# Optimization experiments

Hardware: AMD Instinct MI355X
Metric: run time of the kernel (lower is better)

## Reference

```python
import jax, jax.numpy as jnp
import numpy as np

N_BUILDINGS = 4096
NUM_CLUSTERS = 128
EMBED_DIM = 128
TEMPORAL_DIM = 24


def setup_inputs() -> dict:
    key = jax.random.key(0)
    ks = jax.random.split(key, 12)
    E, N, C, T = EMBED_DIM, N_BUILDINGS, NUM_CLUSTERS, TEMPORAL_DIM

    def lin(k, fi, fo):
        k1, k2 = jax.random.split(k)
        w = jax.random.normal(k1, (fo, fi), jnp.float32) / np.sqrt(fi).astype(np.float32)
        b = jax.random.normal(k2, (fo,), jnp.float32) * 0.01
        return w, b

    fp_w1, fp_b1 = lin(ks[0], 2 * E + 2, 128)
    fp_w2, fp_b2 = lin(ks[1], 128, 64)
    fp_w3, fp_b3 = lin(ks[2], 64, 1)
    en_w1, en_b1 = lin(ks[3], 1, 16)
    en_w2, en_b2 = lin(ks[4], 16, 1)
    ps_w1, ps_b1 = lin(ks[5], E, 32)
    ps_w2, ps_b2 = lin(ks[6], 32, 1)

    embeddings = jax.random.normal(ks[7], (1, N, E), jnp.float32)
    generation = jax.random.uniform(ks[8], (1, N, T), jnp.float32) * 50.0
    consumption = jax.random.uniform(ks[9], (1, N, T), jnp.float32) * 50.0
    positions = jax.random.uniform(ks[10], (1, N, 2), jnp.float32) * 1000.0
    cluster_assignments = (jnp.arange(N) % C)[None, :].astype(jnp.int32)

    return dict(embeddings=embeddings, generation=generation, consumption=consumption,
                positions=positions,
                fp_w1=fp_w1, fp_b1=fp_b1, fp_w2=fp_w2, fp_b2=fp_b2, fp_w3=fp_w3, fp_b3=fp_b3,
                en_w1=en_w1, en_b1=en_b1, en_w2=en_w2, en_b2=en_b2,
                ps_w1=ps_w1, ps_b1=ps_b1, ps_w2=ps_w2, ps_b2=ps_b2,
                cluster_assignments=cluster_assignments, num_clusters=C, current_hour=12)


def _greedy_cluster(net0, prio, effm, pf):
    """Greedy allocation within one cluster. net0,prio: [K]; effm,pf: [K,K].
    Surplus rows and deficit cols are both visited in descending priority order;
    non-surplus rows have avail=0 and non-deficit cols have needed<=0, matching the
    original code's subset selection + break/continue semantics."""
    K = net0.shape[0]
    order = jnp.argsort(-prio)
    inv = jnp.argsort(order)
    net_o = net0[order]
    eff_o = effm[order][:, order]
    pf_o = pf[order][:, order]

    def outer(dnet, i):
        avail0 = jnp.maximum(net_o[i], 0.0)  # surplus net is never mutated

        def inner(carry, j):
            avail, dn = carry
            needed = -dn[j]
            active = (avail > 0.0) & (needed > 0.0)
            f = jnp.where(active, jnp.minimum(jnp.minimum(avail, needed), pf_o[i, j]), 0.0)
            dn = dn.at[j].add(f * eff_o[i, j])  # deficit receives delivered flow
            return (avail - f, dn), (f, active)

        (_, dnet), (frow, arow) = jax.lax.scan(inner, (avail0, dnet), jnp.arange(K))
        return dnet, (frow, arow)

    dnet, (flows_o, act_o) = jax.lax.scan(outer, net_o, jnp.arange(K))
    return flows_o[inv][:, inv], act_o[inv][:, inv], dnet[inv]


def _forward(embeddings, generation, consumption, positions,
             fp_w1, fp_b1, fp_w2, fp_b2, fp_w3, fp_b3,
             en_w1, en_b1, en_w2, en_b2,
             ps_w1, ps_b1, ps_w2, ps_b2,
             cluster_assignments, num_clusters, current_hour):
    B, N, E = embeddings.shape
    C = num_clusters
    K = N // C
    net = generation[0, :, current_hour] - consumption[0, :, current_hour]  # [N]

    g = jnp.argsort(cluster_assignments[0]).reshape(C, K)  # [C,K] building ids per cluster
    emb_c = embeddings[0][g]   # [C,K,E]
    pos_c = positions[0][g]    # [C,K,2]
    net_c = net[g]             # [C,K]

    # priority scorer (eval mode)
    h = jax.nn.relu(emb_c @ ps_w1.T + ps_b1)
    prio_c = jax.nn.sigmoid(h @ ps_w2.T + ps_b2)[..., 0]  # [C,K]

    # pairwise distances within cluster
    dist = jnp.linalg.norm(pos_c[:, :, None, :] - pos_c[:, None, :, :], axis=-1)  # [C,K,K]

    # efficiency net: eff = 0.85 + 0.13*sigmoid(MLP(dist/1000))
    eh = jax.nn.relu((dist / 1000.0)[..., None] * en_w1[:, 0] + en_b1)  # [C,K,K,16]
    eff = 0.85 + 0.13 * jax.nn.sigmoid(eh @ en_w2.T + en_b2)[..., 0]    # [C,K,K]

    # flow predictor on concat([emb_i, emb_j, dist, hour/24]); split W1 to avoid
    # materializing the [C,K,K,2E+2] feature tensor. Dropout is eval-mode identity.
    W1a, W1b = fp_w1[:, :E], fp_w1[:, E:2 * E]
    w1d, w1h = fp_w1[:, 2 * E], fp_w1[:, 2 * E + 1]
    hi = emb_c @ W1a.T  # [C,K,128]
    hj = emb_c @ W1b.T  # [C,K,128]
    hour_f = current_hour / 24.0
    h1 = jax.nn.relu(hi[:, :, None, :] + hj[:, None, :, :] + dist[..., None] * w1d + hour_f * w1h + fp_b1)
    h2 = jax.nn.relu(h1 @ fp_w2.T + fp_b2)
    pflow = jax.nn.softplus(h2 @ fp_w3.T + fp_b3)[..., 0]  # [C,K,K]

    flows_c, act_c, dnet_c = jax.vmap(_greedy_cluster)(net_c, prio_c, eff, pflow)

    sharing = jnp.zeros((N, N), embeddings.dtype).at[g[:, :, None], g[:, None, :]].set(flows_c)
    effmat = jnp.ones((N, N), embeddings.dtype).at[g[:, :, None], g[:, None, :]].set(
        jnp.where(act_c, eff, 1.0))
    net_after = jnp.zeros((N,), embeddings.dtype).at[g].set(dnet_c)

    sharing = sharing[None]
    effmat = effmat[None]
    total_shared = sharing.sum()
    energy_sent = sharing.sum(axis=2)
    energy_received = (sharing * effmat).sum(axis=1)
    return sharing, effmat, total_shared, energy_sent, energy_received, net_after[None]


def reference(embeddings, generation, consumption, positions,
              fp_w1, fp_b1, fp_w2, fp_b2, fp_w3, fp_b3,
              en_w1, en_b1, en_w2, en_b2,
              ps_w1, ps_b1, ps_w2, ps_b2,
              cluster_assignments, num_clusters, current_hour):
    return _forward(embeddings, generation, consumption, positions,
                    fp_w1, fp_b1, fp_w2, fp_b2, fp_w3, fp_b3,
                    en_w1, en_b1, en_w2, en_b2,
                    ps_w1, ps_b1, ps_w2, ps_b2,
                    cluster_assignments, num_clusters, current_hour)
```

## Files before the change

### kernel.cpp

```cpp
#include <hip/hip_runtime.h>
#include <math.h>

#define NB 4096
#define NC 128
#define NK 32
#define NE 128

typedef __bf16 bf16x8 __attribute__((ext_vector_type(8)));
typedef float floatx4 __attribute__((ext_vector_type(4)));

__device__ __forceinline__ float sigmoidf_(float x){
  if (x >= 0.f){ float z = expf(-x); return 1.f/(1.f+z); }
  float z = expf(x); return z/(1.f+z);
}
__device__ __forceinline__ float softplusf_(float x){
  return fmaxf(x, 0.f) + log1pf(expf(-fabsf(x)));
}
__device__ __forceinline__ unsigned int pack_bf16(float a, float b){
  unsigned short ua = __builtin_bit_cast(unsigned short, (__bf16)a);
  unsigned short ub = __builtin_bit_cast(unsigned short, (__bf16)b);
  return (unsigned int)ua | ((unsigned int)ub << 16);
}

__global__ void k_prep_group(const float* __restrict__ fp_w1, const float* __restrict__ ps_w1,
                             const float* __restrict__ fp_b1, const float* __restrict__ fp_w2,
                             const int* __restrict__ assign, const int* __restrict__ hourp,
                             float* __restrict__ w1at, float* __restrict__ w1bt,
                             float* __restrict__ ps_w1t, int* __restrict__ g,
                             int* __restrict__ row_of, float* __restrict__ w1d_c,
                             float* __restrict__ bzc, uint4* __restrict__ w2f,
                             float* __restrict__ total){
  int bid = blockIdx.x;
  int t = threadIdx.x;
  if (bid < 80){
    int idx = bid*256 + t;
    if (idx < 128*128){
      int o = idx >> 7, e = idx & 127;
      w1at[e*128 + o] = fp_w1[o*258 + e];
      w1bt[e*128 + o] = fp_w1[o*258 + 128 + e];
    } else {
      int i2 = idx - 128*128;
      if (i2 < 128*32){
        int e = i2 >> 5, q = i2 & 31;
        ps_w1t[e*32 + q] = ps_w1[q*128 + e];
      }
    }
  } else if (bid < 96){
    __shared__ int hist[NC];
    __shared__ int loc[256];
    int start = (bid - 80)*256;
    for (int c = t; c < NC; c += 256) hist[c] = 0;
    __syncthreads();
    for (int j = t; j < start; j += 256) atomicAdd(&hist[assign[j]], 1);
    int i = start + t;
    int c = assign[i];
    loc[t] = c;
    __syncthreads();
    int r = hist[c];
    for (int j = 0; j < 256; ++j) r += (j < t && loc[j] == c) ? 1 : 0;
    if (r >= NK) r = NK - 1;
    g[c*NK + r] = i;
    row_of[i] = c*NK + r;
  } else if (bid == 96){
    if (t < 128){
      float hour_f = (float)hourp[0] / 24.0f;
      w1d_c[t] = fp_w1[t*258 + 256];
      bzc[t]   = fmaf(hour_f, fp_w1[t*258 + 257], fp_b1[t]);
    }
    if (t == 128) total[0] = 0.f;
  } else {
    for (int ff = t; ff < 1024; ff += 256){
      int lane = ff & 63, fi = ff >> 6;
      int nt = fi >> 2, ks = fi & 3;
      int o = nt*16 + (lane & 15);
      int kb = ks*32 + (lane >> 4)*8;
      const float* src = fp_w2 + o*128 + kb;
      uint4 u;
      u.x = pack_bf16(src[0], src[1]);
      u.y = pack_bf16(src[2], src[3]);
      u.z = pack_bf16(src[4], src[5]);
      u.w = pack_bf16(src[6], src[7]);
      w2f[ff] = u;
    }
  }
}

__global__ void k_prio(const float* __restrict__ emb, const float* __restrict__ gen,
                       const float* __restrict__ cons, const float* __restrict__ pos,
                       const float* __restrict__ ps_w1t, const float* __restrict__ ps_b1,
                       const float* __restrict__ ps_w2, const float* __restrict__ ps_b2,
                       const int* __restrict__ row_of, const int* __restrict__ hourp,
                       float* __restrict__ net_c, float* __restrict__ prio_c,
                       float* __restrict__ pos_c){
  __shared__ float es[8*128];
  __shared__ float ws[128*32];
  int t = threadIdx.x;
  int i0 = blockIdx.x*8;
  for (int idx = t; idx < 8*128; idx += 256) es[idx] = emb[i0*128 + idx];
  for (int idx = t; idx < 128*32; idx += 256) ws[idx] = ps_w1t[idx];
  __syncthreads();
  int bl = t >> 5, q = t & 31;
  int i = i0 + bl;
  float acc = ps_b1[q];
  const float* er = &es[bl*128];
  for (int e = 0; e < 128; ++e) acc = fmaf(er[e], ws[e*32 + q], acc);
  float v = fmaxf(acc, 0.f) * ps_w2[q];
  for (int m = 16; m >= 1; m >>= 1) v += __shfl_xor(v, m, 32);
  if (q == 0){
    int ck = row_of[i];
    prio_c[ck] = sigmoidf_(v + ps_b2[0]);
    int h = hourp[0];
    net_c[ck] = gen[i*24 + h] - cons[i*24 + h];
    pos_c[2*ck]   = pos[2*i];
    pos_c[2*ck+1] = pos[2*i+1];
  }
}

__global__ void k_hij(const float* __restrict__ emb, const float* __restrict__ w1at,
                      const float* __restrict__ w1bt, const int* __restrict__ row_of,
                      float* __restrict__ hi_c, float* __restrict__ hj_c){
  __shared__ float es[16*132];
  int t = threadIdx.x;
  int i0 = blockIdx.x*16;
  for (int idx = t; idx < 16*128; idx += 256){
    int b = idx >> 7, e = idx & 127;
    es[b*132 + e] = emb[(i0 + b)*128 + e];
  }
  __syncthreads();
  int o = t & 127, half = t >> 7;
  float ai[8], aj[8];
#pragma unroll
  for (int r = 0; r < 8; ++r){ ai[r] = 0.f; aj[r] = 0.f; }
  for (int e = 0; e < 128; e += 4){
    float wa0 = w1at[(e+0)*128 + o], wa1 = w1at[(e+1)*128 + o];
    float wa2 = w1at[(e+2)*128 + o], wa3 = w1at[(e+3)*128 + o];
    float wb0 = w1bt[(e+0)*128 + o], wb1 = w1bt[(e+1)*128 + o];
    float wb2 = w1bt[(e+2)*128 + o], wb3 = w1bt[(e+3)*128 + o];
#pragma unroll
    for (int r = 0; r < 8; ++r){
      float4 ev = *(const float4*)&es[(half*8 + r)*132 + e];
      ai[r] = fmaf(ev.x, wa0, fmaf(ev.y, wa1, fmaf(ev.z, wa2, fmaf(ev.w, wa3, ai[r]))));
      aj[r] = fmaf(ev.x, wb0, fmaf(ev.y, wb1, fmaf(ev.z, wb2, fmaf(ev.w, wb3, aj[r]))));
    }
  }
#pragma unroll
  for (int r = 0; r < 8; ++r){
    int b = i0 + half*8 + r;
    int ck = row_of[b];
    hi_c[ck*128 + o] = ai[r];
    hj_c[ck*128 + o] = aj[r];
  }
}

__global__ __launch_bounds__(256) void k_pflow(
    const float* __restrict__ hi_c, const float* __restrict__ hj_c,
    const float* __restrict__ pos_c, const float* __restrict__ w1d_c,
    const float* __restrict__ bzc, const uint4* __restrict__ w2f,
    const float* __restrict__ fp_b2, const float* __restrict__ fp_w3,
    const float* __restrict__ fp_b3, float* __restrict__ pflow){
  int t = threadIdx.x;
  int lane = t & 63, wv = t >> 6;
  int gw = blockIdx.x*4 + wv;
  int c = gw >> 6;
  int rem = gw & 63;
  int i = rem >> 1, j0 = (rem & 1)*16;
  int l16 = lane & 15, quad = lane >> 4;
  int j = j0 + l16;
  float xi = pos_c[(c*NK + i)*2 + 0], yi = pos_c[(c*NK + i)*2 + 1];
  float xj = pos_c[(c*NK + j)*2 + 0], yj = pos_c[(c*NK + j)*2 + 1];
  float dx = xi - xj, dy = yi - yj;
  float d = sqrtf(fmaf(dx, dx, dy*dy));
  const float4* hi4 = (const float4*)(hi_c + (c*NK + i)*128);
  const float4* hj4 = (const float4*)(hj_c + (c*NK + j)*128);
  const float4* wd4 = (const float4*)w1d_c;
  const float4* bz4 = (const float4*)bzc;
  bf16x8 af[4];
#pragma unroll
  for (int ks = 0; ks < 4; ++ks){
    int q8 = ks*8 + quad*2;
    float4 a0 = hi4[q8], a1 = hi4[q8 + 1];
    float4 b0 = hj4[q8], b1 = hj4[q8 + 1];
    float4 w0 = wd4[q8], w1 = wd4[q8 + 1];
    float4 z0 = bz4[q8], z1 = bz4[q8 + 1];
    float v0 = fmaxf(a0.x + b0.x + fmaf(d, w0.x, z0.x), 0.f);
    float v1 = fmaxf(a0.y + b0.y + fmaf(d, w0.y, z0.y), 0.f);
    float v2 = fmaxf(a0.z + b0.z + fmaf(d, w0.z, z0.z), 0.f);
    float v3 = fmaxf(a0.w + b0.w + fmaf(d, w0.w, z0.w), 0.f);
    float v4 = fmaxf(a1.x + b1.x + fmaf(d, w1.x, z1.x), 0.f);
    float v5 = fmaxf(a1.y + b1.y + fmaf(d, w1.y, z1.y), 0.f);
    float v6 = fmaxf(a1.z + b1.z + fmaf(d, w1.z, z1.z), 0.f);
    float v7 = fmaxf(a1.w + b1.w + fmaf(d, w1.w, z1.w), 0.f);
    uint4 u;
    u.x = pack_bf16(v0, v1);
    u.y = pack_bf16(v2, v3);
    u.z = pack_bf16(v4, v5);
    u.w = pack_bf16(v6, v7);
    af[ks] = __builtin_bit_cast(bf16x8, u);
  }
  bf16x8 bfr[4][4];
#pragma unroll
  for (int nt = 0; nt < 4; ++nt)
#pragma unroll
    for (int ks = 0; ks < 4; ++ks)
      bfr[nt][ks] = __builtin_bit_cast(bf16x8, w2f[(nt*4 + ks)*64 + lane]);
  floatx4 acc[4];
#pragma unroll
  for (int nt = 0; nt < 4; ++nt){
    acc[nt] = (floatx4){0.f, 0.f, 0.f, 0.f};
#pragma unroll
    for (int ks = 0; ks < 4; ++ks)
      acc[nt] = __builtin_amdgcn_mfma_f32_16x16x32_bf16(af[ks], bfr[nt][ks], acc[nt], 0, 0, 0);
  }
  float b2v[4], w3v[4];
#pragma unroll
  for (int nt = 0; nt < 4; ++nt){
    b2v[nt] = fp_b2[nt*16 + l16];
    w3v[nt] = fp_w3[nt*16 + l16];
  }
  float b3 = fp_b3[0];
#pragma unroll
  for (int r = 0; r < 4; ++r){
    float s = 0.f;
#pragma unroll
    for (int nt = 0; nt < 4; ++nt)
      s = fmaf(fmaxf(acc[nt][r] + b2v[nt], 0.f), w3v[nt], s);
#pragma unroll
    for (int m = 8; m >= 1; m >>= 1) s += __shfl_xor(s, m);
    if (l16 == 0)
      pflow[c*1024 + i*32 + j0 + quad*4 + r] = softplusf_(s + b3);
  }
}

__global__ __launch_bounds__(64) void k_greedy(
    const float* __restrict__ net_c, const float* __restrict__ prio_c,
    const float* __restrict__ pos_c, const float* __restrict__ en_w1,
    const float* __restrict__ en_b1, const float* __restrict__ en_w2,
    const float* __restrict__ en_b2, const float* __restrict__ pflow,
    const int* __restrict__ g,
    float* __restrict__ fl_c, float* __restrict__ ef_c, float* __restrict__ total,
    float* __restrict__ esent, float* __restrict__ erecv, float* __restrict__ nafter){
  __shared__ float pf_s[1024];
  __shared__ float ef_s[1024];
  __shared__ float fl_s[1024];
  __shared__ float efm_s[1024];
  __shared__ float px[32], py[32];
  __shared__ int order_s[32];
  __shared__ int gl[32];
  int t = threadIdx.x;
  int tl = t & 31;
  int c = blockIdx.x;
  for (int e = t; e < 1024; e += 64) pf_s[e] = pflow[c*1024 + e];
  if (t < 32){
    float2 p2 = ((const float2*)pos_c)[c*NK + t];
    px[t] = p2.x; py[t] = p2.y;
    gl[t] = g[c*NK + t];
  }
  __syncthreads();
  for (int e = t; e < 1024; e += 64){
    int ii = e >> 5, jj = e & 31;
    float dx = px[ii] - px[jj], dy = py[ii] - py[jj];
    float d = sqrtf(fmaf(dx, dx, dy*dy));
    float ds = d * (1.0f/1000.0f);
    float acc = en_b2[0];
#pragma unroll
    for (int q = 0; q < 16; ++q)
      acc = fmaf(fmaxf(fmaf(ds, en_w1[q], en_b1[q]), 0.f), en_w2[q], acc);
    ef_s[e] = 0.85f + 0.13f*sigmoidf_(acc);
  }
  float p = (t < 32) ? prio_c[c*NK + t] : -1e30f;
  int rank = 0;
  for (int k = 0; k < 32; ++k){
    float pk = __shfl(p, k, 32);
    rank += ((pk > p) || (pk == p && k < tl)) ? 1 : 0;
  }
  if (t < 32) order_s[rank] = t;
  __syncthreads();
  int b = order_s[tl];
  float net0 = net_c[c*NK + b];
  float dnet = net0;
  float recv = 0.f;
  float ctotal = 0.f;
  for (int i = 0; i < 32; ++i){
    int a = order_s[i];
    float av0 = fmaxf(__shfl(net0, i, 32), 0.f);
    float pf = pf_s[a*32 + b];
    float ef = ef_s[a*32 + b];
    float needed = -dnet;
    float m = (needed > 0.f) ? fminf(needed, pf) : 0.f;
    float s = m;
#pragma unroll
    for (int dd = 1; dd < 32; dd <<= 1){
      float u = __shfl_up(s, dd, 32);
      if (tl >= dd) s += u;
    }
    float Se = __shfl_up(s, 1, 32);
    if (tl == 0) Se = 0.f;
    float rprev = fmaxf(av0 - Se, 0.f);
    int act = (rprev > 0.f) && (needed > 0.f);
    float f = fminf(m, rprev);
    dnet = fmaf(f, ef, dnet);
    recv = fmaf(f, ef, recv);
    if (t < 32){
      fl_s[a*32 + b]  = f;
      efm_s[a*32 + b] = act ? ef : 1.0f;
    }
    float rs = f;
    for (int mm = 16; mm >= 1; mm >>= 1) rs += __shfl_xor(rs, mm, 32);
    if (t == 0){ esent[gl[a]] = rs; ctotal += rs; }
  }
  if (t < 32){
    nafter[gl[b]] = dnet;
    erecv[gl[b]]  = recv;
  }
  if (t == 0) atomicAdd(total, ctotal);
  __syncthreads();
  for (int e = t; e < 1024; e += 64){
    fl_c[c*1024 + e] = fl_s[e];
    ef_c[c*1024 + e] = efm_s[e];
  }
}

__global__ __launch_bounds__(256) void k_write(
    const float* __restrict__ fl_c, const float* __restrict__ ef_c,
    const int* __restrict__ g, const int* __restrict__ row_of,
    float* __restrict__ sharing, float* __restrict__ effm){
  __shared__ float rowS[4096];
  __shared__ float rowE[4096];
  __shared__ int   cols[32];
  __shared__ float vals[32];
  __shared__ float vale[32];
  int t = threadIdx.x;
  int r = blockIdx.x;
  int ra = row_of[r];
  int c = ra >> 5, a = ra & 31;
  if (t < 32){
    cols[t] = g[c*NK + t];
    vals[t] = fl_c[c*1024 + a*32 + t];
    vale[t] = ef_c[c*1024 + a*32 + t];
  }
  float4 z4 = make_float4(0.f, 0.f, 0.f, 0.f);
  float4 o4 = make_float4(1.f, 1.f, 1.f, 1.f);
  float4* s4 = (float4*)rowS;
  float4* e4 = (float4*)rowE;
#pragma unroll
  for (int q = 0; q < 4; ++q){ s4[t + 256*q] = z4; e4[t + 256*q] = o4; }
  __syncthreads();
  if (t < 32){ rowS[cols[t]] = vals[t]; rowE[cols[t]] = vale[t]; }
  __syncthreads();
  float4* gs = (float4*)(sharing + (long)r*NB);
  float4* ge = (float4*)(effm    + (long)r*NB);
#pragma unroll
  for (int q = 0; q < 4; ++q){ gs[t + 256*q] = s4[t + 256*q]; ge[t + 256*q] = e4[t + 256*q]; }
}

extern "C" void kernel_launch(void* const* d_in, const int* in_sizes, int n_in,
                              void* d_out, int out_size, void* d_ws, size_t ws_size,
                              hipStream_t stream){
  (void)in_sizes; (void)n_in; (void)out_size; (void)ws_size;
  const float* emb   = (const float*)d_in[0];
  const float* gen   = (const float*)d_in[1];
  const float* cons  = (const float*)d_in[2];
  const float* pos   = (const float*)d_in[3];
  const float* fp_w1 = (const float*)d_in[4];
  const float* fp_b1 = (const float*)d_in[5];
  const float* fp_w2 = (const float*)d_in[6];
  const float* fp_b2 = (const float*)d_in[7];
  const float* fp_w3 = (const float*)d_in[8];
  const float* fp_b3 = (const float*)d_in[9];
  const float* en_w1 = (const float*)d_in[10];
  const float* en_b1 = (const float*)d_in[11];
  const float* en_w2 = (const float*)d_in[12];
  const float* en_b2 = (const float*)d_in[13];
  const float* ps_w1 = (const float*)d_in[14];
  const float* ps_b1 = (const float*)d_in[15];
  const float* ps_w2 = (const float*)d_in[16];
  const float* ps_b2 = (const float*)d_in[17];
  const int*   assign = (const int*)d_in[18];
  const int*   hourp  = (const int*)d_in[20];

  char* ws = (char*)d_ws;
  float* w1at   = (float*)(ws + 0);
  float* w1bt   = (float*)(ws + 65536);
  float* ps_w1t = (float*)(ws + 131072);
  int*   g      = (int*)  (ws + 147456);
  int*   row_of = (int*)  (ws + 163840);
  float* net_c  = (float*)(ws + 180224);
  float* prio_c = (float*)(ws + 196608);
  float* pos_c  = (float*)(ws + 212992);
  float* w1d_c  = (float*)(ws + 245760);
  float* bzc    = (float*)(ws + 246272);
  float* hi_c   = (float*)(ws + 262144);
  float* hj_c   = (float*)(ws + 2359296);
  float* pflow  = (float*)(ws + 4456448);
  float* fl_c   = (float*)(ws + 4980736);
  float* ef_c   = (float*)(ws + 5505024);
  uint4* w2f    = (uint4*)(ws + 6029312);

  float* sharing = (float*)d_out;
  float* effm    = sharing + (long)NB*NB;
  float* total   = effm + (long)NB*NB;
  float* esent   = total + 1;
  float* erecv   = esent + NB;
  float* nafter  = erecv + NB;

  hipLaunchKernelGGL(k_prep_group, dim3(98), dim3(256), 0, stream,
                     fp_w1, ps_w1, fp_b1, fp_w2, assign, hourp,
                     w1at, w1bt, ps_w1t, g, row_of, w1d_c, bzc, w2f, total);
  hipLaunchKernelGGL(k_prio, dim3(512), dim3(256), 0, stream,
                     emb, gen, cons, pos, ps_w1t, ps_b1, ps_w2, ps_b2,
                     row_of, hourp, net_c, prio_c, pos_c);
  hipLaunchKernelGGL(k_hij, dim3(256), dim3(256), 0, stream,
                     emb, w1at, w1bt, row_of, hi_c, hj_c);
  hipLaunchKernelGGL(k_pflow, dim3(2048), dim3(256), 0, stream,
                     hi_c, hj_c, pos_c, w1d_c, bzc, w2f, fp_b2, fp_w3, fp_b3,
                     pflow);
  hipLaunchKernelGGL(k_greedy, dim3(128), dim3(64), 0, stream,
                     net_c, prio_c, pos_c, en_w1, en_b1, en_w2, en_b2, pflow, g,
                     fl_c, ef_c, total, esent, erecv, nafter);
  hipLaunchKernelGGL(k_write, dim3(4096), dim3(256), 0, stream,
                     fl_c, ef_c, g, row_of, sharing, effm);
}
```

Baseline: 267.5 us.

## Fuse all stages into one cooperative persistent kernel with grid syncs

Replaces the six separate launches with a single cooperative kernel of 512 blocks that runs the prep, hidden projections, priority, pairwise MLP, greedy and scatter-write stages, separated by grid-wide syncs. Blocks loop over work that previously had its own grid size: 4 iterations for pflow, 8 rows each for the write stage, and the greedy stage runs on a subset of blocks with 64 active threads. This removes per-kernel launch overhead and the gaps between launches. In exchange it adds grid-sync cost, limits occupancy to the co-resident grid, and leaves most blocks idle during the serial greedy phase. The dominant cost, writing two 4096x4096 matrices, is unchanged.

```diff
diff --git a/kernel.cpp b/kernel.cpp
--- a/kernel.cpp
+++ b/kernel.cpp
@@ -1,5 +1,8 @@
 #include <hip/hip_runtime.h>
+#include <hip/hip_cooperative_groups.h>
 #include <math.h>
+
+namespace cg = cooperative_groups;
 
 #define NB 4096
 #define NC 128
@@ -22,401 +25,384 @@
   return (unsigned int)ua | ((unsigned int)ub << 16);
 }
 
-__global__ void k_prep_group(const float* __restrict__ fp_w1, const float* __restrict__ ps_w1,
-                             const float* __restrict__ fp_b1, const float* __restrict__ fp_w2,
-                             const int* __restrict__ assign, const int* __restrict__ hourp,
-                             float* __restrict__ w1at, float* __restrict__ w1bt,
-                             float* __restrict__ ps_w1t, int* __restrict__ g,
-                             int* __restrict__ row_of, float* __restrict__ w1d_c,
-                             float* __restrict__ bzc, uint4* __restrict__ w2f,
-                             float* __restrict__ total){
+struct KParams {
+  const float *emb, *gen, *cons, *pos;
+  const float *fp_w1, *fp_b1, *fp_w2, *fp_b2, *fp_w3, *fp_b3;
+  const float *en_w1, *en_b1, *en_w2, *en_b2;
+  const float *ps_w1, *ps_b1, *ps_w2, *ps_b2;
+  const int *assign, *hourp;
+  float *w1at, *w1bt, *ps_w1t;
+  int *g, *row_of;
+  float *w1d_c, *bzc;
+  uint4 *w2f;
+  float *net_c, *prio_c, *pos_c;
+  float *hi_c, *hj_c, *pflow, *fl_c, *ef_c;
+  float *sharing, *effm, *total, *esent, *erecv, *nafter;
+};
+
+__global__ __launch_bounds__(256, 4) void k_fused(KParams p){
+  __shared__ __align__(16) char smem_raw[33536];
+  cg::grid_group grid = cg::this_grid();
+  int t = threadIdx.x;
   int bid = blockIdx.x;
-  int t = threadIdx.x;
+  int lane = t & 63, wv = t >> 6;
+
   if (bid < 80){
     int idx = bid*256 + t;
     if (idx < 128*128){
       int o = idx >> 7, e = idx & 127;
-      w1at[e*128 + o] = fp_w1[o*258 + e];
-      w1bt[e*128 + o] = fp_w1[o*258 + 128 + e];
+      p.w1at[e*128 + o] = p.fp_w1[o*258 + e];
+      p.w1bt[e*128 + o] = p.fp_w1[o*258 + 128 + e];
     } else {
       int i2 = idx - 128*128;
       if (i2 < 128*32){
         int e = i2 >> 5, q = i2 & 31;
-        ps_w1t[e*32 + q] = ps_w1[q*128 + e];
+        p.ps_w1t[e*32 + q] = p.ps_w1[q*128 + e];
       }
     }
   } else if (bid < 96){
-    __shared__ int hist[NC];
-    __shared__ int loc[256];
+    int* hist = (int*)smem_raw;
+    int* loc  = hist + NC;
     int start = (bid - 80)*256;
     for (int c = t; c < NC; c += 256) hist[c] = 0;
     __syncthreads();
-    for (int j = t; j < start; j += 256) atomicAdd(&hist[assign[j]], 1);
+    for (int j = t; j < start; j += 256) atomicAdd(&hist[p.assign[j]], 1);
     int i = start + t;
-    int c = assign[i];
+    int c = p.assign[i];
     loc[t] = c;
     __syncthreads();
     int r = hist[c];
     for (int j = 0; j < 256; ++j) r += (j < t && loc[j] == c) ? 1 : 0;
     if (r >= NK) r = NK - 1;
-    g[c*NK + r] = i;
-    row_of[i] = c*NK + r;
+    p.g[c*NK + r] = i;
+    p.row_of[i] = c*NK + r;
   } else if (bid == 96){
     if (t < 128){
-      float hour_f = (float)hourp[0] / 24.0f;
-      w1d_c[t] = fp_w1[t*258 + 256];
-      bzc[t]   = fmaf(hour_f, fp_w1[t*258 + 257], fp_b1[t]);
-    }
-    if (t == 128) total[0] = 0.f;
-  } else {
+      float hour_f = (float)p.hourp[0] / 24.0f;
+      p.w1d_c[t] = p.fp_w1[t*258 + 256];
+      p.bzc[t]   = fmaf(hour_f, p.fp_w1[t*258 + 257], p.fp_b1[t]);
+    }
+    if (t == 128) p.total[0] = 0.f;
+  } else if (bid == 97){
     for (int ff = t; ff < 1024; ff += 256){
-      int lane = ff & 63, fi = ff >> 6;
+      int ln = ff & 63, fi = ff >> 6;
       int nt = fi >> 2, ks = fi & 3;
-      int o = nt*16 + (lane & 15);
-      int kb = ks*32 + (lane >> 4)*8;
-      const float* src = fp_w2 + o*128 + kb;
+      int o = nt*16 + (ln & 15);
+      int kb = ks*32 + (ln >> 4)*8;
+      const float* src = p.fp_w2 + o*128 + kb;
       uint4 u;
       u.x = pack_bf16(src[0], src[1]);
       u.y = pack_bf16(src[2], src[3]);
       u.z = pack_bf16(src[4], src[5]);
       u.w = pack_bf16(src[6], src[7]);
-      w2f[ff] = u;
-    }
-  }
-}
-
-__global__ void k_prio(const float* __restrict__ emb, const float* __restrict__ gen,
-                       const float* __restrict__ cons, const float* __restrict__ pos,
-                       const float* __restrict__ ps_w1t, const float* __restrict__ ps_b1,
-                       const float* __restrict__ ps_w2, const float* __restrict__ ps_b2,
-                       const int* __restrict__ row_of, const int* __restrict__ hourp,
-                       float* __restrict__ net_c, float* __restrict__ prio_c,
-                       float* __restrict__ pos_c){
-  __shared__ float es[8*128];
-  __shared__ float ws[128*32];
-  int t = threadIdx.x;
-  int i0 = blockIdx.x*8;
-  for (int idx = t; idx < 8*128; idx += 256) es[idx] = emb[i0*128 + idx];
-  for (int idx = t; idx < 128*32; idx += 256) ws[idx] = ps_w1t[idx];
+      p.w2f[ff] = u;
+    }
+  }
+  __threadfence();
+  grid.sync();
+
+  {
+    float* es = (float*)smem_raw;
+    int i0 = bid*8;
+    for (int idx = t; idx < 8*128; idx += 256){
+      int b = idx >> 7, e = idx & 127;
+      es[b*132 + e] = p.emb[(i0 + b)*128 + e];
+    }
+    __syncthreads();
+    int o = t & 127, half = t >> 7;
+    float ai[4], aj[4];
+#pragma unroll
+    for (int r = 0; r < 4; ++r){ ai[r] = 0.f; aj[r] = 0.f; }
+    for (int e = 0; e < 128; e += 4){
+      float wa0 = p.w1at[(e+0)*128 + o], wa1 = p.w1at[(e+1)*128 + o];
+      float wa2 = p.w1at[(e+2)*128 + o], wa3 = p.w1at[(e+3)*128 + o];
+      float wb0 = p.w1bt[(e+0)*128 + o], wb1 = p.w1bt[(e+1)*128 + o];
+      float wb2 = p.w1bt[(e+2)*128 + o], wb3 = p.w1bt[(e+3)*128 + o];
+#pragma unroll
+      for (int r = 0; r < 4; ++r){
+        float4 ev = *(const float4*)&es[(half*4 + r)*132 + e];
+        ai[r] = fmaf(ev.x, wa0, fmaf(ev.y, wa1, fmaf(ev.z, wa2, fmaf(ev.w, wa3, ai[r]))));
+        aj[r] = fmaf(ev.x, wb0, fmaf(ev.y, wb1, fmaf(ev.z, wb2, fmaf(ev.w, wb3, aj[r]))));
+      }
+    }
+#pragma unroll
+    for (int r = 0; r < 4; ++r){
+      int b = i0 + half*4 + r;
+      int ck = p.row_of[b];
+      p.hi_c[ck*128 + o] = ai[r];
+      p.hj_c[ck*128 + o] = aj[r];
+    }
+  }
   __syncthreads();
-  int bl = t >> 5, q = t & 31;
-  int i = i0 + bl;
-  float acc = ps_b1[q];
-  const float* er = &es[bl*128];
-  for (int e = 0; e < 128; ++e) acc = fmaf(er[e], ws[e*32 + q], acc);
-  float v = fmaxf(acc, 0.f) * ps_w2[q];
-  for (int m = 16; m >= 1; m >>= 1) v += __shfl_xor(v, m, 32);
-  if (q == 0){
-    int ck = row_of[i];
-    prio_c[ck] = sigmoidf_(v + ps_b2[0]);
-    int h = hourp[0];
-    net_c[ck] = gen[i*24 + h] - cons[i*24 + h];
-    pos_c[2*ck]   = pos[2*i];
-    pos_c[2*ck+1] = pos[2*i+1];
-  }
-}
-
-__global__ void k_hij(const float* __restrict__ emb, const float* __restrict__ w1at,
-                      const float* __restrict__ w1bt, const int* __restrict__ row_of,
-                      float* __restrict__ hi_c, float* __restrict__ hj_c){
-  __shared__ float es[16*132];
-  int t = threadIdx.x;
-  int i0 = blockIdx.x*16;
-  for (int idx = t; idx < 16*128; idx += 256){
-    int b = idx >> 7, e = idx & 127;
-    es[b*132 + e] = emb[(i0 + b)*128 + e];
-  }
-  __syncthreads();
-  int o = t & 127, half = t >> 7;
-  float ai[8], aj[8];
-#pragma unroll
-  for (int r = 0; r < 8; ++r){ ai[r] = 0.f; aj[r] = 0.f; }
-  for (int e = 0; e < 128; e += 4){
-    float wa0 = w1at[(e+0)*128 + o], wa1 = w1at[(e+1)*128 + o];
-    float wa2 = w1at[(e+2)*128 + o], wa3 = w1at[(e+3)*128 + o];
-    float wb0 = w1bt[(e+0)*128 + o], wb1 = w1bt[(e+1)*128 + o];
-    float wb2 = w1bt[(e+2)*128 + o], wb3 = w1bt[(e+3)*128 + o];
-#pragma unroll
-    for (int r = 0; r < 8; ++r){
-      float4 ev = *(const float4*)&es[(half*8 + r)*132 + e];
-      ai[r] = fmaf(ev.x, wa0, fmaf(ev.y, wa1, fmaf(ev.z, wa2, fmaf(ev.w, wa3, ai[r]))));
-      aj[r] = fmaf(ev.x, wb0, fmaf(ev.y, wb1, fmaf(ev.z, wb2, fmaf(ev.w, wb3, aj[r]))));
-    }
-  }
-#pragma unroll
-  for (int r = 0; r < 8; ++r){
-    int b = i0 + half*8 + r;
-    int ck = row_of[b];
-    hi_c[ck*128 + o] = ai[r];
-    hj_c[ck*128 + o] = aj[r];
-  }
-}
-
-__global__ __launch_bounds__(256) void k_pflow(
-    const float* __restrict__ hi_c, const float* __restrict__ hj_c,
-    const float* __restrict__ pos_c, const float* __restrict__ w1d_c,
-    const float* __restrict__ bzc, const uint4* __restrict__ w2f,
-    const float* __restrict__ fp_b2, const float* __restrict__ fp_w3,
-    const float* __restrict__ fp_b3, float* __restrict__ pflow){
-  int t = threadIdx.x;
-  int lane = t & 63, wv = t >> 6;
-  int gw = blockIdx.x*4 + wv;
-  int c = gw >> 6;
-  int rem = gw & 63;
-  int i = rem >> 1, j0 = (rem & 1)*16;
-  int l16 = lane & 15, quad = lane >> 4;
-  int j = j0 + l16;
-  float xi = pos_c[(c*NK + i)*2 + 0], yi = pos_c[(c*NK + i)*2 + 1];
-  float xj = pos_c[(c*NK + j)*2 + 0], yj = pos_c[(c*NK + j)*2 + 1];
-  float dx = xi - xj, dy = yi - yj;
-  float d = sqrtf(fmaf(dx, dx, dy*dy));
-  const float4* hi4 = (const float4*)(hi_c + (c*NK + i)*128);
-  const float4* hj4 = (const float4*)(hj_c + (c*NK + j)*128);
-  const float4* wd4 = (const float4*)w1d_c;
-  const float4* bz4 = (const float4*)bzc;
-  bf16x8 af[4];
-#pragma unroll
-  for (int ks = 0; ks < 4; ++ks){
-    int q8 = ks*8 + quad*2;
-    float4 a0 = hi4[q8], a1 = hi4[q8 + 1];
-    float4 b0 = hj4[q8], b1 = hj4[q8 + 1];
-    float4 w0 = wd4[q8], w1 = wd4[q8 + 1];
-    float4 z0 = bz4[q8], z1 = bz4[q8 + 1];
-    float v0 = fmaxf(a0.x + b0.x + fmaf(d, w0.x, z0.x), 0.f);
-    float v1 = fmaxf(a0.y + b0.y + fmaf(d, w0.y, z0.y), 0.f);
-    float v2 = fmaxf(a0.z + b0.z + fmaf(d, w0.z, z0.z), 0.f);
-    float v3 = fmaxf(a0.w + b0.w + fmaf(d, w0.w, z0.w), 0.f);
-    float v4 = fmaxf(a1.x + b1.x + fmaf(d, w1.x, z1.x), 0.f);
-    float v5 = fmaxf(a1.y + b1.y + fmaf(d, w1.y, z1.y), 0.f);
-    float v6 = fmaxf(a1.z + b1.z + fmaf(d, w1.z, z1.z), 0.f);
-    float v7 = fmaxf(a1.w + b1.w + fmaf(d, w1.w, z1.w), 0.f);
-    uint4 u;
-    u.x = pack_bf16(v0, v1);
-    u.y = pack_bf16(v2, v3);
-    u.z = pack_bf16(v4, v5);
-    u.w = pack_bf16(v6, v7);
-    af[ks] = __builtin_bit_cast(bf16x8, u);
-  }
-  bf16x8 bfr[4][4];
-#pragma unroll
-  for (int nt = 0; nt < 4; ++nt)
-#pragma unroll
-    for (int ks = 0; ks < 4; ++ks)
-      bfr[nt][ks] = __builtin_bit_cast(bf16x8, w2f[(nt*4 + ks)*64 + lane]);
-  floatx4 acc[4];
-#pragma unroll
-  for (int nt = 0; nt < 4; ++nt){
-    acc[nt] = (floatx4){0.f, 0.f, 0.f, 0.f};
-#pragma unroll
-    for (int ks = 0; ks < 4; ++ks)
-      acc[nt] = __builtin_amdgcn_mfma_f32_16x16x32_bf16(af[ks], bfr[nt][ks], acc[nt], 0, 0, 0);
-  }
-  float b2v[4], w3v[4];
-#pragma unroll
-  for (int nt = 0; nt < 4; ++nt){
-    b2v[nt] = fp_b2[nt*16 + l16];
-    w3v[nt] = fp_w3[nt*16 + l16];
-  }
-  float b3 = fp_b3[0];
-#pragma unroll
-  for (int r = 0; r < 4; ++r){
-    float s = 0.f;
+
+  {
+    float* es2 = (float*)smem_raw;
+    float* wsm = es2 + 1024;
+    int i0 = bid*8;
+    for (int idx = t; idx < 8*128; idx += 256) es2[idx] = p.emb[i0*128 + idx];
+    for (int idx = t; idx < 128*32; idx += 256) wsm[idx] = p.ps_w1t[idx];
+    __syncthreads();
+    int bl = t >> 5, q = t & 31;
+    int i = i0 + bl;
+    float acc = p.ps_b1[q];
+    const float* er = &es2[bl*128];
+    for (int e = 0; e < 128; ++e) acc = fmaf(er[e], wsm[e*32 + q], acc);
+    float v = fmaxf(acc, 0.f) * p.ps_w2[q];
+    for (int m = 16; m >= 1; m >>= 1) v += __shfl_xor(v, m, 32);
+    if (q == 0){
+      int ck = p.row_of[i];
+      p.prio_c[ck] = sigmoidf_(v + p.ps_b2[0]);
+      int h = p.hourp[0];
+      p.net_c[ck] = p.gen[i*24 + h] - p.cons[i*24 + h];
+      p.pos_c[2*ck]   = p.pos[2*i];
+      p.pos_c[2*ck+1] = p.pos[2*i+1];
+    }
+  }
+  __threadfence();
+  grid.sync();
+
+  {
+    int l16 = lane & 15, quad = lane >> 4;
+    bf16x8 bfr[4][4];
 #pragma unroll
     for (int nt = 0; nt < 4; ++nt)
-      s = fmaf(fmaxf(acc[nt][r] + b2v[nt], 0.f), w3v[nt], s);
-#pragma unroll
-    for (int m = 8; m >= 1; m >>= 1) s += __shfl_xor(s, m);
-    if (l16 == 0)
-      pflow[c*1024 + i*32 + j0 + quad*4 + r] = softplusf_(s + b3);
-  }
-}
-
-__global__ __launch_bounds__(64) void k_greedy(
-    const float* __restrict__ net_c, const float* __restrict__ prio_c,
-    const float* __restrict__ pos_c, const float* __restrict__ en_w1,
-    const float* __restrict__ en_b1, const float* __restrict__ en_w2,
-    const float* __restrict__ en_b2, const float* __restrict__ pflow,
-    const int* __restrict__ g,
-    float* __restrict__ fl_c, float* __restrict__ ef_c, float* __restrict__ total,
-    float* __restrict__ esent, float* __restrict__ erecv, float* __restrict__ nafter){
-  __shared__ float pf_s[1024];
-  __shared__ float ef_s[1024];
-  __shared__ float fl_s[1024];
-  __shared__ float efm_s[1024];
-  __shared__ float px[32], py[32];
-  __shared__ int order_s[32];
-  __shared__ int gl[32];
-  int t = threadIdx.x;
-  int tl = t & 31;
-  int c = blockIdx.x;
-  for (int e = t; e < 1024; e += 64) pf_s[e] = pflow[c*1024 + e];
-  if (t < 32){
-    float2 p2 = ((const float2*)pos_c)[c*NK + t];
-    px[t] = p2.x; py[t] = p2.y;
-    gl[t] = g[c*NK + t];
-  }
-  __syncthreads();
-  for (int e = t; e < 1024; e += 64){
-    int ii = e >> 5, jj = e & 31;
-    float dx = px[ii] - px[jj], dy = py[ii] - py[jj];
-    float d = sqrtf(fmaf(dx, dx, dy*dy));
-    float ds = d * (1.0f/1000.0f);
-    float acc = en_b2[0];
-#pragma unroll
-    for (int q = 0; q < 16; ++q)
-      acc = fmaf(fmaxf(fmaf(ds, en_w1[q], en_b1[q]), 0.f), en_w2[q], acc);
-    ef_s[e] = 0.85f + 0.13f*sigmoidf_(acc);
-  }
-  float p = (t < 32) ? prio_c[c*NK + t] : -1e30f;
-  int rank = 0;
-  for (int k = 0; k < 32; ++k){
-    float pk = __shfl(p, k, 32);
-    rank += ((pk > p) || (pk == p && k < tl)) ? 1 : 0;
-  }
-  if (t < 32) order_s[rank] = t;
-  __syncthreads();
-  int b = order_s[tl];
-  float net0 = net_c[c*NK + b];
-  float dnet = net0;
-  float recv = 0.f;
-  float ctotal = 0.f;
-  for (int i = 0; i < 32; ++i){
-    int a = order_s[i];
-    float av0 = fmaxf(__shfl(net0, i, 32), 0.f);
-    float pf = pf_s[a*32 + b];
-    float ef = ef_s[a*32 + b];
-    float needed = -dnet;
-    float m = (needed > 0.f) ? fminf(needed, pf) : 0.f;
-    float s = m;
-#pragma unroll
-    for (int dd = 1; dd < 32; dd <<= 1){
-      float u = __shfl_up(s, dd, 32);
-      if (tl >= dd) s += u;
-    }
-    float Se = __shfl_up(s, 1, 32);
-    if (tl == 0) Se = 0.f;
-    float rprev = fmaxf(av0 - Se, 0.f);
-    int act = (rprev > 0.f) && (needed > 0.f);
-    float f = fminf(m, rprev);
-    dnet = fmaf(f, ef, dnet);
-    recv = fmaf(f, ef, recv);
+#pragma unroll
+      for (int ks = 0; ks < 4; ++ks)
+        bfr[nt][ks] = __builtin_bit_cast(bf16x8, p.w2f[(nt*4 + ks)*64 + lane]);
+    float b2v[4], w3v[4];
+#pragma unroll
+    for (int nt = 0; nt < 4; ++nt){
+      b2v[nt] = p.fp_b2[nt*16 + l16];
+      w3v[nt] = p.fp_w3[nt*16 + l16];
+    }
+    float b3 = p.fp_b3[0];
+    for (int it = 0; it < 4; ++it){
+      int gw = it*2048 + bid*4 + wv;
+      int c = gw >> 6;
+      int rem = gw & 63;
+      int i = rem >> 1, j0 = (rem & 1)*16;
+      int j = j0 + l16;
+      float xi = p.pos_c[(c*NK + i)*2 + 0], yi = p.pos_c[(c*NK + i)*2 + 1];
+      float xj = p.pos_c[(c*NK + j)*2 + 0], yj = p.pos_c[(c*NK + j)*2 + 1];
+      float dx = xi - xj, dy = yi - yj;
+      float d = sqrtf(fmaf(dx, dx, dy*dy));
+      const float4* hi4 = (const float4*)(p.hi_c + (c*NK + i)*128);
+      const float4* hj4 = (const float4*)(p.hj_c + (c*NK + j)*128);
+      const float4* wd4 = (const float4*)p.w1d_c;
+      const float4* bz4 = (const float4*)p.bzc;
+      bf16x8 af[4];
+#pragma unroll
+      for (int ks = 0; ks < 4; ++ks){
+        int q8 = ks*8 + quad*2;
+        float4 a0 = hi4[q8], a1 = hi4[q8 + 1];
+        float4 b0 = hj4[q8], b1 = hj4[q8 + 1];
+        float4 w0 = wd4[q8], w1 = wd4[q8 + 1];
+        float4 z0 = bz4[q8], z1 = bz4[q8 + 1];
+        float v0 = fmaxf(a0.x + b0.x + fmaf(d, w0.x, z0.x), 0.f);
+        float v1 = fmaxf(a0.y + b0.y + fmaf(d, w0.y, z0.y), 0.f);
+        float v2 = fmaxf(a0.z + b0.z + fmaf(d, w0.z, z0.z), 0.f);
+        float v3 = fmaxf(a0.w + b0.w + fmaf(d, w0.w, z0.w), 0.f);
+        float v4 = fmaxf(a1.x + b1.x + fmaf(d, w1.x, z1.x), 0.f);
+        float v5 = fmaxf(a1.y + b1.y + fmaf(d, w1.y, z1.y), 0.f);
+        float v6 = fmaxf(a1.z + b1.z + fmaf(d, w1.z, z1.z), 0.f);
+        float v7 = fmaxf(a1.w + b1.w + fmaf(d, w1.w, z1.w), 0.f);
+        uint4 u;
+        u.x = pack_bf16(v0, v1);
+        u.y = pack_bf16(v2, v3);
+        u.z = pack_bf16(v4, v5);
+        u.w = pack_bf16(v6, v7);
+        af[ks] = __builtin_bit_cast(bf16x8, u);
+      }
+      floatx4 acc[4];
+#pragma unroll
+      for (int nt = 0; nt < 4; ++nt){
+        acc[nt] = (floatx4){0.f, 0.f, 0.f, 0.f};
+#pragma unroll
+        for (int ks = 0; ks < 4; ++ks)
+          acc[nt] = __builtin_amdgcn_mfma_f32_16x16x32_bf16(af[ks], bfr[nt][ks], acc[nt], 0, 0, 0);
+      }
+#pragma unroll
+      for (int r = 0; r < 4; ++r){
+        float s = 0.f;
+#pragma unroll
+        for (int nt = 0; nt < 4; ++nt)
+          s = fmaf(fmaxf(acc[nt][r] + b2v[nt], 0.f), w3v[nt], s);
+#pragma unroll
+        for (int m = 8; m >= 1; m >>= 1) s += __shfl_xor(s, m);
+        if (l16 == 0)
+          p.pflow[c*1024 + i*32 + j0 + quad*4 + r] = softplusf_(s + b3);
+      }
+    }
+  }
+  __threadfence();
+  grid.sync();
+
+  if (bid < 128){
+    float* pf_s = (float*)smem_raw;
+    float* ef_s = pf_s + 1024;
+    float* px = ef_s + 1024;
+    float* py = px + 32;
+    int* gl = (int*)(py + 32);
+    int* order_s = gl + 32;
+    int c = bid;
+    for (int e = t; e < 1024; e += 256) pf_s[e] = p.pflow[c*1024 + e];
     if (t < 32){
-      fl_s[a*32 + b]  = f;
-      efm_s[a*32 + b] = act ? ef : 1.0f;
-    }
-    float rs = f;
-    for (int mm = 16; mm >= 1; mm >>= 1) rs += __shfl_xor(rs, mm, 32);
-    if (t == 0){ esent[gl[a]] = rs; ctotal += rs; }
-  }
-  if (t < 32){
-    nafter[gl[b]] = dnet;
-    erecv[gl[b]]  = recv;
-  }
-  if (t == 0) atomicAdd(total, ctotal);
-  __syncthreads();
-  for (int e = t; e < 1024; e += 64){
-    fl_c[c*1024 + e] = fl_s[e];
-    ef_c[c*1024 + e] = efm_s[e];
-  }
-}
-
-__global__ __launch_bounds__(256) void k_write(
-    const float* __restrict__ fl_c, const float* __restrict__ ef_c,
-    const int* __restrict__ g, const int* __restrict__ row_of,
-    float* __restrict__ sharing, float* __restrict__ effm){
-  __shared__ float rowS[4096];
-  __shared__ float rowE[4096];
-  __shared__ int   cols[32];
-  __shared__ float vals[32];
-  __shared__ float vale[32];
-  int t = threadIdx.x;
-  int r = blockIdx.x;
-  int ra = row_of[r];
-  int c = ra >> 5, a = ra & 31;
-  if (t < 32){
-    cols[t] = g[c*NK + t];
-    vals[t] = fl_c[c*1024 + a*32 + t];
-    vale[t] = ef_c[c*1024 + a*32 + t];
-  }
-  float4 z4 = make_float4(0.f, 0.f, 0.f, 0.f);
-  float4 o4 = make_float4(1.f, 1.f, 1.f, 1.f);
-  float4* s4 = (float4*)rowS;
-  float4* e4 = (float4*)rowE;
-#pragma unroll
-  for (int q = 0; q < 4; ++q){ s4[t + 256*q] = z4; e4[t + 256*q] = o4; }
-  __syncthreads();
-  if (t < 32){ rowS[cols[t]] = vals[t]; rowE[cols[t]] = vale[t]; }
-  __syncthreads();
-  float4* gs = (float4*)(sharing + (long)r*NB);
-  float4* ge = (float4*)(effm    + (long)r*NB);
-#pragma unroll
-  for (int q = 0; q < 4; ++q){ gs[t + 256*q] = s4[t + 256*q]; ge[t + 256*q] = e4[t + 256*q]; }
+      float2 p2 = ((const float2*)p.pos_c)[c*NK + t];
+      px[t] = p2.x; py[t] = p2.y;
+      gl[t] = p.g[c*NK + t];
+    }
+    __syncthreads();
+    for (int e = t; e < 1024; e += 256){
+      int ii = e >> 5, jj = e & 31;
+      float dx = px[ii] - px[jj], dy = py[ii] - py[jj];
+      float d = sqrtf(fmaf(dx, dx, dy*dy));
+      float ds = d * (1.0f/1000.0f);
+      float acc = p.en_b2[0];
+#pragma unroll
+      for (int q = 0; q < 16; ++q)
+        acc = fmaf(fmaxf(fmaf(ds, p.en_w1[q], p.en_b1[q]), 0.f), p.en_w2[q], acc);
+      ef_s[e] = 0.85f + 0.13f*sigmoidf_(acc);
+    }
+    if (t < 64){
+      int tl = t & 31;
+      float pr = (t < 32) ? p.prio_c[c*NK + t] : -1e30f;
+      int rank = 0;
+      for (int k = 0; k < 32; ++k){
+        float pk = __shfl(pr, k, 32);
+        rank += ((pk > pr) || (pk == pr && k < tl)) ? 1 : 0;
+      }
+      if (t < 32) order_s[rank] = t;
+    }
+    __syncthreads();
+    if (t < 64){
+      int tl = t & 31;
+      int b = order_s[tl];
+      float net0 = p.net_c[c*NK + b];
+      float dnet = net0;
+      float recv = 0.f;
+      float ctotal = 0.f;
+      for (int i = 0; i < 32; ++i){
+        int a = order_s[i];
+        float av0 = fmaxf(__shfl(net0, i, 32), 0.f);
+        float pf = pf_s[a*32 + b];
+        float ef = ef_s[a*32 + b];
+        float needed = -dnet;
+        float m = (needed > 0.f) ? fminf(needed, pf) : 0.f;
+        float s = m;
+#pragma unroll
+        for (int dd = 1; dd < 32; dd <<= 1){
+          float u = __shfl_up(s, dd, 32);
+          if (tl >= dd) s += u;
+        }
+        float Se = __shfl_up(s, 1, 32);
+        if (tl == 0) Se = 0.f;
+        float rprev = fmaxf(av0 - Se, 0.f);
+        int act = (rprev > 0.f) && (needed > 0.f);
+        float f = fminf(m, rprev);
+        dnet = fmaf(f, ef, dnet);
+        recv = fmaf(f, ef, recv);
+        if (t < 32){
+          p.fl_c[c*1024 + a*32 + b] = f;
+          p.ef_c[c*1024 + a*32 + b] = act ? ef : 1.0f;
+        }
+        float rs = f;
+        for (int mm = 16; mm >= 1; mm >>= 1) rs += __shfl_xor(rs, mm, 32);
+        if (t == 0){ p.esent[gl[a]] = rs; ctotal += rs; }
+      }
+      if (t < 32){
+        p.nafter[gl[b]] = dnet;
+        p.erecv[gl[b]]  = recv;
+      }
+      if (t == 0) atomicAdd(p.total, ctotal);
+    }
+  }
+  __threadfence();
+  grid.sync();
+
+  {
+    float* rowS = (float*)smem_raw;
+    float* rowE = rowS + 4096;
+    int* cols = (int*)(rowE + 4096);
+    float* vals = (float*)(cols + 32);
+    float* vale = vals + 32;
+    float4 z4 = make_float4(0.f, 0.f, 0.f, 0.f);
+    float4 o4 = make_float4(1.f, 1.f, 1.f, 1.f);
+    float4* s4 = (float4*)rowS;
+    float4* e4 = (float4*)rowE;
+    for (int rr = 0; rr < 8; ++rr){
+      int r = bid*8 + rr;
+      int ra = p.row_of[r];
+      int c2 = ra >> 5, a = ra & 31;
+      if (t < 32){
+        cols[t] = p.g[c2*NK + t];
+        vals[t] = p.fl_c[c2*1024 + a*32 + t];
+        vale[t] = p.ef_c[c2*1024 + a*32 + t];
+      }
+#pragma unroll
+      for (int q = 0; q < 4; ++q){ s4[t + 256*q] = z4; e4[t + 256*q] = o4; }
+      __syncthreads();
+      if (t < 32){ rowS[cols[t]] = vals[t]; rowE[cols[t]] = vale[t]; }
+      __syncthreads();
+      float4* gs = (float4*)(p.sharing + (long)r*NB);
+      float4* ge = (float4*)(p.effm    + (long)r*NB);
+#pragma unroll
+      for (int q = 0; q < 4; ++q){ gs[t + 256*q] = s4[t + 256*q]; ge[t + 256*q] = e4[t + 256*q]; }
+      __syncthreads();
+    }
+  }
 }
 
 extern "C" void kernel_launch(void* const* d_in, const int* in_sizes, int n_in,
                               void* d_out, int out_size, void* d_ws, size_t ws_size,
                               hipStream_t stream){
   (void)in_sizes; (void)n_in; (void)out_size; (void)ws_size;
-  const float* emb   = (const float*)d_in[0];
-  const float* gen   = (const float*)d_in[1];
-  const float* cons  = (const float*)d_in[2];
-  const float* pos   = (const float*)d_in[3];
-  const float* fp_w1 = (const float*)d_in[4];
-  const float* fp_b1 = (const float*)d_in[5];
-  const float* fp_w2 = (const float*)d_in[6];
-  const float* fp_b2 = (const float*)d_in[7];
-  const float* fp_w3 = (const float*)d_in[8];
-  const float* fp_b3 = (const float*)d_in[9];
-  const float* en_w1 = (const float*)d_in[10];
-  const float* en_b1 = (const float*)d_in[11];
-  const float* en_w2 = (const float*)d_in[12];
-  const float* en_b2 = (const float*)d_in[13];
-  const float* ps_w1 = (const float*)d_in[14];
-  const float* ps_b1 = (const float*)d_in[15];
-  const float* ps_w2 = (const float*)d_in[16];
-  const float* ps_b2 = (const float*)d_in[17];
-  const int*   assign = (const int*)d_in[18];
-  const int*   hourp  = (const int*)d_in[20];
+  KParams prm;
+  prm.emb   = (const float*)d_in[0];
+  prm.gen   = (const float*)d_in[1];
+  prm.cons  = (const float*)d_in[2];
+  prm.pos   = (const float*)d_in[3];
+  prm.fp_w1 = (const float*)d_in[4];
+  prm.fp_b1 = (const float*)d_in[5];
+  prm.fp_w2 = (const float*)d_in[6];
+  prm.fp_b2 = (const float*)d_in[7];
+  prm.fp_w3 = (const float*)d_in[8];
+  prm.fp_b3 = (const float*)d_in[9];
+  prm.en_w1 = (const float*)d_in[10];
+  prm.en_b1 = (const float*)d_in[11];
+  prm.en_w2 = (const float*)d_in[12];
+  prm.en_b2 = (const float*)d_in[13];
+  prm.ps_w1 = (const float*)d_in[14];
+  prm.ps_b1 = (const float*)d_in[15];
+  prm.ps_w2 = (const float*)d_in[16];
+  prm.ps_b2 = (const float*)d_in[17];
+  prm.assign = (const int*)d_in[18];
+  prm.hourp  = (const int*)d_in[20];
 
   char* ws = (char*)d_ws;
-  float* w1at   = (float*)(ws + 0);
-  float* w1bt   = (float*)(ws + 65536);
-  float* ps_w1t = (float*)(ws + 131072);
-  int*   g      = (int*)  (ws + 147456);
-  int*   row_of = (int*)  (ws + 163840);
-  float* net_c  = (float*)(ws + 180224);
-  float* prio_c = (float*)(ws + 196608);
-  float* pos_c  = (float*)(ws + 212992);
-  float* w1d_c  = (float*)(ws + 245760);
-  float* bzc    = (float*)(ws + 246272);
-  float* hi_c   = (float*)(ws + 262144);
-  float* hj_c   = (float*)(ws + 2359296);
-  float* pflow  = (float*)(ws + 4456448);
-  float* fl_c   = (float*)(ws + 4980736);
-  float* ef_c   = (float*)(ws + 5505024);
-  uint4* w2f    = (uint4*)(ws + 6029312);
-
-  float* sharing = (float*)d_out;
-  float* effm    = sharing + (long)NB*NB;
-  float* total   = effm + (long)NB*NB;
-  float* esent   = total + 1;
-  float* erecv   = esent + NB;
-  float* nafter  = erecv + NB;
-
-  hipLaunchKernelGGL(k_prep_group, dim3(98), dim3(256), 0, stream,
-                     fp_w1, ps_w1, fp_b1, fp_w2, assign, hourp,
-                     w1at, w1bt, ps_w1t, g, row_of, w1d_c, bzc, w2f, total);
-  hipLaunchKernelGGL(k_prio, dim3(512), dim3(256), 0, stream,
-                     emb, gen, cons, pos, ps_w1t, ps_b1, ps_w2, ps_b2,
-                     row_of, hourp, net_c, prio_c, pos_c);
-  hipLaunchKernelGGL(k_hij, dim3(256), dim3(256), 0, stream,
-                     emb, w1at, w1bt, row_of, hi_c, hj_c);
-  hipLaunchKernelGGL(k_pflow, dim3(2048), dim3(256), 0, stream,
-                     hi_c, hj_c, pos_c, w1d_c, bzc, w2f, fp_b2, fp_w3, fp_b3,
-                     pflow);
-  hipLaunchKernelGGL(k_greedy, dim3(128), dim3(64), 0, stream,
-                     net_c, prio_c, pos_c, en_w1, en_b1, en_w2, en_b2, pflow, g,
-                     fl_c, ef_c, total, esent, erecv, nafter);
-  hipLaunchKernelGGL(k_write, dim3(4096), dim3(256), 0, stream,
-                     fl_c, ef_c, g, row_of, sharing, effm);
+  prm.w1at   = (float*)(ws + 0);
+  prm.w1bt   = (float*)(ws + 65536);
+  prm.ps_w1t = (float*)(ws + 131072);
+  prm.g      = (int*)  (ws + 147456);
+  prm.row_of = (int*)  (ws + 163840);
+  prm.net_c  = (float*)(ws + 180224);
+  prm.prio_c = (float*)(ws + 196608);
+  prm.pos_c  = (float*)(ws + 212992);
+  prm.w1d_c  = (float*)(ws + 245760);
+  prm.bzc    = (float*)(ws + 246272);
+  prm.w2f    = (uint4*)(ws + 262144);
+  prm.hi_c   = (float*)(ws + 524288);
+  prm.hj_c   = (float*)(ws + 2621440);
+  prm.pflow  = (float*)(ws + 4718592);
+  prm.fl_c   = (float*)(ws + 5242880);
+  prm.ef_c   = (float*)(ws + 5767168);
+
+  prm.sharing = (float*)d_out;
+  prm.effm    = prm.sharing + (long)NB*NB;
+  prm.total   = prm.effm + (long)NB*NB;
+  prm.esent   = prm.total + 1;
+  prm.erecv   = prm.esent + NB;
+  prm.nafter  = prm.erecv + NB;
+
+  void* args[] = { &prm };
+  hipLaunchCooperativeKernel((void*)k_fused, dim3(512), dim3(256), args, 0, stream);
 }
```

Result: slower. 643.5 us (+140.5%).
